# Performance work log

Hardware: AMD Instinct MI355X
Metric: run time of the kernel (lower is better)

## Reference

```python
import jax, jax.numpy as jnp
import numpy as np

B, T, D, BOT = 4, 4096, 2048, 256


def setup_inputs() -> dict:
    key = jax.random.key(0)
    k1, k2, k3, k4 = jax.random.split(key, 4)
    return {
        "hdc_chars": jax.random.normal(k1, (B, T, D), dtype=jnp.float32),
        "decay_matrix": jax.random.uniform(k2, (B, T, T), dtype=jnp.float32),
        "Wq": jax.random.normal(k3, (BOT, D), dtype=jnp.float32) * (D ** -0.5),
        "bq": jnp.zeros((BOT,), dtype=jnp.float32),
        "Wk": jax.random.normal(k4, (BOT, D), dtype=jnp.float32) * (D ** -0.5),
        "bk": jnp.zeros((BOT,), dtype=jnp.float32),
    }


def reference(hdc_chars, decay_matrix, Wq, bq, Wk, bk):
    # hdc_chars: [B,T,D]; decay_matrix: [B,T,T]
    bot = Wq.shape[0]
    scale = bot ** -0.5
    q = hdc_chars @ Wq.T + bq          # [B,T,bot]
    k = hdc_chars @ Wk.T + bk          # [B,T,bot]
    scores = jnp.einsum("btc,bsc->bts", q, k) * scale  # [B,T,T]
    t = scores.shape[-1]
    i = jnp.arange(t)[:, None]
    j = jnp.arange(t)[None, :]
    allowed = j <= i - 4               # tril(diagonal=-4): blocks local echo
    scores = jnp.where(allowed, scores, jnp.float32(-65000.0))
    resonance = jax.nn.softmax(scores, axis=-1)
    combined = 0.7 * decay_matrix + 0.3 * resonance
    return combined @ hdc_chars        # [B,T,D]
```

## Files before the change

### kernel.cpp

```cpp
#include <hip/hip_runtime.h>
#include <hip/hip_bf16.h>

#define BB 4
#define TT 4096
#define DD 2048
#define BOTC 256

typedef __bf16 bf16;
typedef __attribute__((ext_vector_type(4))) __bf16 bf16x4;
typedef __attribute__((ext_vector_type(8))) __bf16 bf16x8;
typedef __attribute__((ext_vector_type(4))) float f32x4;

constexpr int BM = 128, BN = 128, BK = 64;

__device__ __forceinline__ void async16(const void* g, bf16* l) {
  __builtin_amdgcn_global_load_lds((const __attribute__((address_space(1))) void*)g,
                                   (__attribute__((address_space(3))) void*)l, 16, 0, 0);
}

#define SBAR asm volatile("s_barrier" ::: "memory")
#define WAIT_LGKM0 asm volatile("s_waitcnt lgkmcnt(0)" ::: "memory")
#define WAIT_VM6 asm volatile("s_waitcnt vmcnt(6)" ::: "memory")
#define WAIT_VM0 asm volatile("s_waitcnt vmcnt(0)" ::: "memory")

template <int EPI>
__global__ __launch_bounds__(256) void gemm_bt(
    const bf16* __restrict__ A, const bf16* __restrict__ Bm, void* __restrict__ Cout,
    const float* __restrict__ bias, int M, int N, int K, int ldA, int ldB,
    long sAb, long sBb, long sCb, float scale) {
  const int b = blockIdx.z;
  const int m0 = blockIdx.y * BM;
  const int n0 = blockIdx.x * BN;
  const int tid = threadIdx.x;
  const int lane = tid & 63;
  const int w = tid >> 6;
  const int wm = (w >> 1) * 64;
  const int wn = (w & 1) * 64;

  if (EPI == 2 && n0 > m0) return;

  __shared__ bf16 As[BM * BK];
  __shared__ bf16 Bs[BN * BK];

  f32x4 acc[4][4] = {};

  const bf16* Arow = A + (size_t)b * sAb + (size_t)m0 * ldA;
  const bf16* Brow = Bm + (size_t)b * sBb + (size_t)n0 * ldB;

  for (int k0 = 0; k0 < K; k0 += BK) {
#pragma unroll
    for (int j = 0; j < 4; ++j) {
      int c = j * 256 + tid;
      int row = c >> 3, kc = c & 7;
      int gk = kc ^ (row & 7);
      async16(Arow + (size_t)row * ldA + k0 + gk * 8, As + (size_t)c * 8);
      async16(Brow + (size_t)row * ldB + k0 + gk * 8, Bs + (size_t)c * 8);
    }
    __syncthreads();
    bf16x8 af[4][2], bfr[4][2];
#pragma unroll
    for (int mi = 0; mi < 4; ++mi)
#pragma unroll
      for (int kk = 0; kk < 2; ++kk) {
        int row = wm + mi * 16 + (lane & 15);
        int kc = kk * 4 + (lane >> 4);
        af[mi][kk] = *(const bf16x8*)(As + ((size_t)row * 8 + (kc ^ (row & 7))) * 8);
      }
#pragma unroll
    for (int ni = 0; ni < 4; ++ni)
#pragma unroll
      for (int kk = 0; kk < 2; ++kk) {
        int row = wn + ni * 16 + (lane & 15);
        int kc = kk * 4 + (lane >> 4);
        bfr[ni][kk] = *(const bf16x8*)(Bs + ((size_t)row * 8 + (kc ^ (row & 7))) * 8);
      }
#pragma unroll
    for (int kk = 0; kk < 2; ++kk)
#pragma unroll
      for (int mi = 0; mi < 4; ++mi)
#pragma unroll
        for (int ni = 0; ni < 4; ++ni)
          acc[mi][ni] = __builtin_amdgcn_mfma_f32_16x16x32_bf16(af[mi][kk], bfr[ni][kk], acc[mi][ni], 0, 0, 0);
    __syncthreads();
  }

  const int lcol = lane & 15;
  const int lrow = (lane >> 4) * 4;

  if (EPI == 1) {
    bf16* C = (bf16*)Cout + (size_t)b * sCb;
#pragma unroll
    for (int mi = 0; mi < 4; ++mi) {
      int rbase = m0 + wm + mi * 16 + lrow;
#pragma unroll
      for (int ni = 0; ni < 4; ++ni) {
        int col = n0 + wn + ni * 16 + lcol;
        float bv = bias[col];
#pragma unroll
        for (int r = 0; r < 4; ++r)
          C[(size_t)(rbase + r) * N + col] = (bf16)(acc[mi][ni][r] + bv);
      }
    }
  } else {
    bf16* C = (bf16*)Cout + (size_t)b * sCb;
#pragma unroll
    for (int mi = 0; mi < 4; ++mi) {
      int rbase = m0 + wm + mi * 16 + lrow;
#pragma unroll
      for (int ni = 0; ni < 4; ++ni) {
        int col = n0 + wn + ni * 16 + lcol;
#pragma unroll
        for (int r = 0; r < 4; ++r) {
          int i = rbase + r;
          float v = acc[mi][ni][r] * scale;
          if (col > i - 4) v = -65000.0f;
          C[(size_t)i * N + col] = (bf16)v;
        }
      }
    }
  }
}

__device__ __forceinline__ void stage_half(const bf16* __restrict__ src, int ld,
                                           bf16* lds, int tid) {
#pragma unroll
  for (int j = 0; j < 2; ++j) {
    int c = j * 512 + tid;
    int row = c >> 3;
    int gk = (c & 7) ^ (row & 7);
    async16(src + (size_t)row * ld + gk * 8, lds + (size_t)c * 8);
  }
}

__device__ __forceinline__ bf16x8 fragrd(const bf16* base, int lr, int kc) {
  return *(const bf16x8*)(base + ((size_t)lr * 8 + (kc ^ (lr & 7))) * 8);
}

__device__ __forceinline__ void load_b4(const bf16* base, int wn, int fr, int fq,
                                        bf16x8 (&bf_)[4][2]) {
#pragma unroll
  for (int ni = 0; ni < 4; ++ni)
#pragma unroll
    for (int kk = 0; kk < 2; ++kk)
      bf_[ni][kk] = fragrd(base, (wn & 1) * 64 + ni * 16 + fr, kk * 4 + fq);
}

__device__ __forceinline__ void load_a4(const bf16* base, int qm, int fr, int fq,
                                        bf16x8 (&a)[4][2]) {
#pragma unroll
  for (int mi = 0; mi < 4; ++mi)
#pragma unroll
    for (int kk = 0; kk < 2; ++kk)
      a[mi][kk] = fragrd(base, qm * 64 + mi * 16 + fr, kk * 4 + fq);
}

__device__ __forceinline__ void mfma_quad(f32x4 (&acc)[8][4], const bf16x8 (&a)[4][2],
                                          const bf16x8 (&bf_)[4][2], int qm, int qn) {
  __builtin_amdgcn_s_setprio(1);
#pragma unroll
  for (int kk = 0; kk < 2; ++kk)
#pragma unroll
    for (int mi = 0; mi < 4; ++mi)
#pragma unroll
      for (int ni = 0; ni < 2; ++ni)
        acc[qm * 4 + mi][qn * 2 + ni] = __builtin_amdgcn_mfma_f32_16x16x32_bf16(
            a[mi][kk], bf_[qn * 2 + ni][kk], acc[qm * 4 + mi][qn * 2 + ni], 0, 0, 0);
  __builtin_amdgcn_s_setprio(0);
}

__global__ __launch_bounds__(512, 2) void gemm256(
    const bf16* __restrict__ A, const bf16* __restrict__ Bm, float* __restrict__ C,
    int N, int K, int ldA, int ldB, long sAb, long sBb, long sCb) {
  const int h = blockIdx.x + 8 * (blockIdx.y + 16 * blockIdx.z);
  const int l = ((h & 7) << 6) + (h >> 3);
  const int bx = l & 7;
  const int lt = l >> 3;
  const int by = lt & 15;
  const int b = lt >> 4;
  const int m0 = by * 256;
  const int n0 = bx * 256;
  const int tid = threadIdx.x;
  const int lane = tid & 63;
  const int w = tid >> 6;
  const int wm = w >> 2;
  const int wn = w & 3;
  const int fr = lane & 15;
  const int fq = lane >> 4;
  const int bh = wn >> 1;
  const int NKT = K >> 6;
  const int NI = K >> 7;

  __shared__ bf16 sA[2][2][8192];
  __shared__ bf16 sB[2][2][8192];

  const bf16* Ab = A + (size_t)b * sAb + (size_t)m0 * ldA;
  const bf16* Bb = Bm + (size_t)b * sBb + (size_t)n0 * ldB;

  f32x4 acc[8][4] = {};
  bf16x8 a[4][2], bf_[4][2];

  stage_half(Bb, ldB, &sB[0][0][0], tid);
  stage_half(Bb + (size_t)128 * ldB, ldB, &sB[0][1][0], tid);
  stage_half(Ab, ldA, &sA[0][0][0], tid);
  stage_half(Ab + (size_t)128 * ldA, ldA, &sA[0][1][0], tid);
  stage_half(Bb + 64, ldB, &sB[1][0][0], tid);
  stage_half(Bb + (size_t)128 * ldB + 64, ldB, &sB[1][1][0], tid);
  stage_half(Ab + 64, ldA, &sA[1][0][0], tid);
  WAIT_VM6;
  SBAR;

  for (int i = 0; i < NI; ++i) {
    const size_t kA1 = (size_t)(2 * i + 1) * 64;
    int t2 = 2 * i + 2; if (t2 > NKT - 1) t2 = NKT - 1;
    int t3 = 2 * i + 3; if (t3 > NKT - 1) t3 = NKT - 1;
    const size_t k2 = (size_t)t2 * 64, k3 = (size_t)t3 * 64;

    load_b4(&sB[0][bh][0], wn, fr, fq, bf_);
    load_a4(&sA[0][wm][0], 0, fr, fq, a);
    stage_half(Ab + (size_t)128 * ldA + kA1, ldA, &sA[1][1][0], tid);
    SBAR; WAIT_LGKM0; __builtin_amdgcn_sched_barrier(0);
    mfma_quad(acc, a, bf_, 0, 0);
    SBAR;
    stage_half(Bb + k2, ldB, &sB[0][0][0], tid);
    SBAR;
    mfma_quad(acc, a, bf_, 0, 1);
    SBAR;
    load_a4(&sA[0][wm][0], 1, fr, fq, a);
    stage_half(Bb + (size_t)128 * ldB + k2, ldB, &sB[0][1][0], tid);
    SBAR; WAIT_LGKM0; __builtin_amdgcn_sched_barrier(0);
    mfma_quad(acc, a, bf_, 1, 0);
    SBAR;
    stage_half(Ab + k2, ldA, &sA[0][0][0], tid);
    SBAR;
    mfma_quad(acc, a, bf_, 1, 1);
    WAIT_VM6;
    SBAR;
    load_b4(&sB[1][bh][0], wn, fr, fq, bf_);
    load_a4(&sA[1][wm][0], 0, fr, fq, a);
    stage_half(Ab + (size_t)128 * ldA + k2, ldA, &sA[0][1][0], tid);
    SBAR; WAIT_LGKM0; __builtin_amdgcn_sched_barrier(0);
    mfma_quad(acc, a, bf_, 0, 0);
    SBAR;
    stage_half(Bb + k3, ldB, &sB[1][0][0], tid);
    SBAR;
    mfma_quad(acc, a, bf_, 0, 1);
    SBAR;
    load_a4(&sA[1][wm][0], 1, fr, fq, a);
    stage_half(Bb + (size_t)128 * ldB + k3, ldB, &sB[1][1][0], tid);
    SBAR; WAIT_LGKM0; __builtin_amdgcn_sched_barrier(0);
    mfma_quad(acc, a, bf_, 1, 0);
    SBAR;
    stage_half(Ab + k3, ldA, &sA[1][0][0], tid);
    SBAR;
    mfma_quad(acc, a, bf_, 1, 1);
    WAIT_VM6;
    SBAR;
  }

  WAIT_VM0;

  float* Cb = C + (size_t)b * sCb;
  const int lrow = fq * 4;
#pragma unroll
  for (int mi = 0; mi < 8; ++mi) {
    int rbase = m0 + wm * 128 + mi * 16 + lrow;
#pragma unroll
    for (int ni = 0; ni < 4; ++ni) {
      int col = n0 + wn * 64 + ni * 16 + fr;
#pragma unroll
      for (int r = 0; r < 4; ++r)
        Cb[(size_t)(rbase + r) * N + col] = acc[mi][ni][r];
    }
  }
}

__global__ __launch_bounds__(256) void conv_transpose(
    const float* __restrict__ hdc, bf16* __restrict__ hb, bf16* __restrict__ hT) {
  __shared__ float tile[64][65];
  int b = blockIdx.z;
  int d0 = blockIdx.x * 64, t0 = blockIdx.y * 64;
  int tid = threadIdx.x;
  const float* src = hdc + (size_t)b * TT * DD;
  bf16* dstb = hb + (size_t)b * TT * DD;
  bf16* dstT = hT + (size_t)b * DD * TT;
  int c4 = tid & 15, r0 = tid >> 4;
#pragma unroll
  for (int rr = 0; rr < 4; ++rr) {
    int r = rr * 16 + r0;
    float4 v = *(const float4*)(src + (size_t)(t0 + r) * DD + d0 + c4 * 4);
    tile[r][c4 * 4 + 0] = v.x;
    tile[r][c4 * 4 + 1] = v.y;
    tile[r][c4 * 4 + 2] = v.z;
    tile[r][c4 * 4 + 3] = v.w;
    bf16x4 o;
    o[0] = (bf16)v.x; o[1] = (bf16)v.y; o[2] = (bf16)v.z; o[3] = (bf16)v.w;
    *(bf16x4*)(dstb + (size_t)(t0 + r) * DD + d0 + c4 * 4) = o;
  }
  __syncthreads();
  int tc = tid & 7, dr0 = tid >> 3;
#pragma unroll
  for (int rr = 0; rr < 2; ++rr) {
    int dr = rr * 32 + dr0;
    bf16x8 o;
#pragma unroll
    for (int e = 0; e < 8; ++e) o[e] = (bf16)tile[tc * 8 + e][dr];
    *(bf16x8*)(dstT + (size_t)(d0 + dr) * TT + t0 + tc * 8) = o;
  }
}

__global__ __launch_bounds__(256) void conv_w(
    const float* __restrict__ Wq, const float* __restrict__ Wk,
    const float* __restrict__ bq, const float* __restrict__ bk,
    bf16* __restrict__ Wqkb, float* __restrict__ bqk) {
  int i = blockIdx.x * 256 + threadIdx.x;
  float4 q = *(const float4*)(Wq + (size_t)i * 4);
  float4 k = *(const float4*)(Wk + (size_t)i * 4);
  bf16x4 qo, ko;
  qo[0] = (bf16)q.x; qo[1] = (bf16)q.y; qo[2] = (bf16)q.z; qo[3] = (bf16)q.w;
  ko[0] = (bf16)k.x; ko[1] = (bf16)k.y; ko[2] = (bf16)k.z; ko[3] = (bf16)k.w;
  *(bf16x4*)(Wqkb + (size_t)i * 4) = qo;
  *(bf16x4*)(Wqkb + (size_t)BOTC * DD + (size_t)i * 4) = ko;
  if (blockIdx.x == 0) {
    bqk[threadIdx.x] = bq[threadIdx.x];
    bqk[256 + threadIdx.x] = bk[threadIdx.x];
  }
}

__global__ __launch_bounds__(256) void softmax_combine(
    bf16* __restrict__ S, const float* __restrict__ decay) {
  int b = blockIdx.y, i = blockIdx.x;
  bf16* srow = S + ((size_t)b * TT + i) * TT;
  const float* drow = decay + ((size_t)b * TT + i) * TT;
  int t = threadIdx.x;
  int lane = t & 63, w = t >> 6;
  const int valid = i - 3;
  const int nc = valid > 0 ? (valid + 7) >> 3 : 0;

  float p[2][8];
  float inv = 0.f, pc = 0.f;

  if (valid > 0) {
    float s[2][8];
#pragma unroll
    for (int u = 0; u < 2; ++u) {
      int c = u * 256 + t;
      if (c < nc) {
        bf16x8 sv = *(const bf16x8*)(srow + (size_t)c * 8);
#pragma unroll
        for (int e = 0; e < 8; ++e) {
          int j = c * 8 + e;
          s[u][e] = j < valid ? (float)sv[e] : -INFINITY;
        }
      } else {
#pragma unroll
        for (int e = 0; e < 8; ++e) s[u][e] = -INFINITY;
      }
    }
    float m = s[0][0];
#pragma unroll
    for (int u = 0; u < 2; ++u)
#pragma unroll
      for (int e = 0; e < 8; ++e) m = fmaxf(m, s[u][e]);
#pragma unroll
    for (int off = 32; off > 0; off >>= 1) m = fmaxf(m, __shfl_xor(m, off));
    __shared__ float redm[4], reds[4];
    if (lane == 0) redm[w] = m;
    __syncthreads();
    m = fmaxf(fmaxf(redm[0], redm[1]), fmaxf(redm[2], redm[3]));

    float sum = 0.f;
#pragma unroll
    for (int u = 0; u < 2; ++u)
#pragma unroll
      for (int e = 0; e < 8; ++e) {
        p[u][e] = __expf(s[u][e] - m);
        sum += p[u][e];
      }
#pragma unroll
    for (int off = 32; off > 0; off >>= 1) sum += __shfl_xor(sum, off);
    if (lane == 0) reds[w] = sum;
    __syncthreads();
    sum = reds[0] + reds[1] + reds[2] + reds[3];
    inv = 0.3f / sum;
  } else {
    pc = 0.3f / 4096.0f;
#pragma unroll
    for (int u = 0; u < 2; ++u)
#pragma unroll
      for (int e = 0; e < 8; ++e) p[u][e] = 0.f;
  }

#pragma unroll
  for (int u = 0; u < 2; ++u) {
    int c = u * 256 + t;
    const float4* d4 = (const float4*)(drow + (size_t)c * 8);
    float4 da = d4[0], db = d4[1];
    float pv[8];
#pragma unroll
    for (int e = 0; e < 8; ++e) pv[e] = p[u][e] * inv + pc;
    bf16x8 o;
    o[0] = (bf16)(0.7f * da.x + pv[0]);
    o[1] = (bf16)(0.7f * da.y + pv[1]);
    o[2] = (bf16)(0.7f * da.z + pv[2]);
    o[3] = (bf16)(0.7f * da.w + pv[3]);
    o[4] = (bf16)(0.7f * db.x + pv[4]);
    o[5] = (bf16)(0.7f * db.y + pv[5]);
    o[6] = (bf16)(0.7f * db.z + pv[6]);
    o[7] = (bf16)(0.7f * db.w + pv[7]);
    *(bf16x8*)(srow + (size_t)c * 8) = o;
  }
}

extern "C" void kernel_launch(void* const* d_in, const int* in_sizes, int n_in,
                              void* d_out, int out_size, void* d_ws, size_t ws_size,
                              hipStream_t stream) {
  (void)in_sizes; (void)n_in; (void)out_size; (void)ws_size;
  const float* hdc = (const float*)d_in[0];
  const float* decay = (const float*)d_in[1];
  const float* Wq = (const float*)d_in[2];
  const float* bq = (const float*)d_in[3];
  const float* Wk = (const float*)d_in[4];
  const float* bk = (const float*)d_in[5];
  float* out = (float*)d_out;

  char* ws = (char*)d_ws;
  bf16* hdc_b = (bf16*)ws; ws += (size_t)BB * TT * DD * 2;
  bf16* hdcT  = (bf16*)ws; ws += (size_t)BB * TT * DD * 2;
  bf16* Wqkb  = (bf16*)ws; ws += (size_t)2 * BOTC * DD * 2;
  float* bqk  = (float*)ws; ws += 2 * BOTC * 4;
  bf16* qk    = (bf16*)ws; ws += (size_t)BB * TT * 2 * BOTC * 2;
  bf16* S     = (bf16*)ws; ws += (size_t)BB * TT * TT * 2;

  conv_transpose<<<dim3(DD / 64, TT / 64, BB), 256, 0, stream>>>(hdc, hdc_b, hdcT);
  conv_w<<<dim3(BOTC * DD / 1024), 256, 0, stream>>>(Wq, Wk, bq, bk, Wqkb, bqk);

  gemm_bt<1><<<dim3((2 * BOTC) / BN, (BB * TT) / BM, 1), 256, 0, stream>>>(
      hdc_b, Wqkb, qk, bqk, BB * TT, 2 * BOTC, DD, DD, DD, 0, 0, 0, 1.0f);

  gemm_bt<2><<<dim3(TT / BN, TT / BM, BB), 256, 0, stream>>>(
      qk, qk + BOTC, S, nullptr, TT, TT, BOTC, 2 * BOTC, 2 * BOTC,
      (long)TT * 2 * BOTC, (long)TT * 2 * BOTC, (long)TT * TT, 0.0625f);

  softmax_combine<<<dim3(TT, BB), 256, 0, stream>>>(S, decay);

  gemm256<<<dim3(DD / 256, TT / 256, BB), 512, 0, stream>>>(
      S, hdcT, out, DD, TT, TT, TT,
      (long)TT * TT, (long)DD * TT, (long)TT * DD);
}
```

Measured before the change: 882.0 us.

## Split B fragment loads into halves and reorder LDS staging schedule in gemm256

Replaces the single 4-fragment B register load with two 2-fragment loads (bq0/bq1) interleaved between MFMA quads. This lowers register pressure and spreads LDS reads across the loop. The async global-to-LDS staging order is reshuffled so that A tiles are prefetched ahead and B tiles are staged inside the iteration, and the vmcnt wait threshold changes from 6 to 4. The aim is better overlap of LDS reads and global loads with MFMA work, at the risk of extra barriers or stalls, or of a hazard if a stage overwrites a buffer still being read.

```diff
diff --git a/kernel.cpp b/kernel.cpp
--- a/kernel.cpp
+++ b/kernel.cpp
@@ -20,7 +20,8 @@
 
 #define SBAR asm volatile("s_barrier" ::: "memory")
 #define WAIT_LGKM0 asm volatile("s_waitcnt lgkmcnt(0)" ::: "memory")
-#define WAIT_VM6 asm volatile("s_waitcnt vmcnt(6)" ::: "memory")
+#define LGKM_HINT8 asm volatile("s_waitcnt lgkmcnt(8)" ::: "memory")
+#define WAIT_VM4 asm volatile("s_waitcnt vmcnt(4)" ::: "memory")
 #define WAIT_VM0 asm volatile("s_waitcnt vmcnt(0)" ::: "memory")
 
 template <int EPI>
@@ -136,13 +137,13 @@
   return *(const bf16x8*)(base + ((size_t)lr * 8 + (kc ^ (lr & 7))) * 8);
 }
 
-__device__ __forceinline__ void load_b4(const bf16* base, int wn, int fr, int fq,
-                                        bf16x8 (&bf_)[4][2]) {
-#pragma unroll
-  for (int ni = 0; ni < 4; ++ni)
+__device__ __forceinline__ void load_b2(const bf16* base, int wn, int fr, int fq,
+                                        int qn, bf16x8 (&bq)[2][2]) {
+#pragma unroll
+  for (int ni = 0; ni < 2; ++ni)
 #pragma unroll
     for (int kk = 0; kk < 2; ++kk)
-      bf_[ni][kk] = fragrd(base, (wn & 1) * 64 + ni * 16 + fr, kk * 4 + fq);
+      bq[ni][kk] = fragrd(base, (wn & 1) * 64 + (qn * 2 + ni) * 16 + fr, kk * 4 + fq);
 }
 
 __device__ __forceinline__ void load_a4(const bf16* base, int qm, int fr, int fq,
@@ -155,7 +156,7 @@
 }
 
 __device__ __forceinline__ void mfma_quad(f32x4 (&acc)[8][4], const bf16x8 (&a)[4][2],
-                                          const bf16x8 (&bf_)[4][2], int qm, int qn) {
+                                          const bf16x8 (&bq)[2][2], int qm, int qn) {
   __builtin_amdgcn_s_setprio(1);
 #pragma unroll
   for (int kk = 0; kk < 2; ++kk)
@@ -164,7 +165,7 @@
 #pragma unroll
       for (int ni = 0; ni < 2; ++ni)
         acc[qm * 4 + mi][qn * 2 + ni] = __builtin_amdgcn_mfma_f32_16x16x32_bf16(
-            a[mi][kk], bf_[qn * 2 + ni][kk], acc[qm * 4 + mi][qn * 2 + ni], 0, 0, 0);
+            a[mi][kk], bq[ni][kk], acc[qm * 4 + mi][qn * 2 + ni], 0, 0, 0);
   __builtin_amdgcn_s_setprio(0);
 }
 
@@ -197,63 +198,66 @@
   const bf16* Bb = Bm + (size_t)b * sBb + (size_t)n0 * ldB;
 
   f32x4 acc[8][4] = {};
-  bf16x8 a[4][2], bf_[4][2];
+  bf16x8 a[4][2], bq0[2][2], bq1[2][2];
 
   stage_half(Bb, ldB, &sB[0][0][0], tid);
   stage_half(Bb + (size_t)128 * ldB, ldB, &sB[0][1][0], tid);
   stage_half(Ab, ldA, &sA[0][0][0], tid);
   stage_half(Ab + (size_t)128 * ldA, ldA, &sA[0][1][0], tid);
-  stage_half(Bb + 64, ldB, &sB[1][0][0], tid);
-  stage_half(Bb + (size_t)128 * ldB + 64, ldB, &sB[1][1][0], tid);
   stage_half(Ab + 64, ldA, &sA[1][0][0], tid);
-  WAIT_VM6;
+  stage_half(Ab + (size_t)128 * ldA + 64, ldA, &sA[1][1][0], tid);
+  WAIT_VM4;
   SBAR;
 
   for (int i = 0; i < NI; ++i) {
-    const size_t kA1 = (size_t)(2 * i + 1) * 64;
+    const size_t k1 = (size_t)(2 * i + 1) * 64;
     int t2 = 2 * i + 2; if (t2 > NKT - 1) t2 = NKT - 1;
     int t3 = 2 * i + 3; if (t3 > NKT - 1) t3 = NKT - 1;
     const size_t k2 = (size_t)t2 * 64, k3 = (size_t)t3 * 64;
 
-    load_b4(&sB[0][bh][0], wn, fr, fq, bf_);
     load_a4(&sA[0][wm][0], 0, fr, fq, a);
-    stage_half(Ab + (size_t)128 * ldA + kA1, ldA, &sA[1][1][0], tid);
-    SBAR; WAIT_LGKM0; __builtin_amdgcn_sched_barrier(0);
-    mfma_quad(acc, a, bf_, 0, 0);
-    SBAR;
+    load_b2(&sB[0][bh][0], wn, fr, fq, 0, bq0);
+    stage_half(Bb + k1, ldB, &sB[1][0][0], tid);
+    LGKM_HINT8;
+    SBAR; WAIT_LGKM0; __builtin_amdgcn_sched_barrier(0);
+    mfma_quad(acc, a, bq0, 0, 0);
+    SBAR;
+    load_b2(&sB[0][bh][0], wn, fr, fq, 1, bq1);
+    stage_half(Bb + (size_t)128 * ldB + k1, ldB, &sB[1][1][0], tid);
+    SBAR; WAIT_LGKM0; __builtin_amdgcn_sched_barrier(0);
+    mfma_quad(acc, a, bq1, 0, 1);
+    SBAR;
+    load_a4(&sA[0][wm][0], 1, fr, fq, a);
     stage_half(Bb + k2, ldB, &sB[0][0][0], tid);
-    SBAR;
-    mfma_quad(acc, a, bf_, 0, 1);
-    SBAR;
-    load_a4(&sA[0][wm][0], 1, fr, fq, a);
+    SBAR; WAIT_LGKM0; __builtin_amdgcn_sched_barrier(0);
+    mfma_quad(acc, a, bq0, 1, 0);
+    SBAR;
     stage_half(Bb + (size_t)128 * ldB + k2, ldB, &sB[0][1][0], tid);
-    SBAR; WAIT_LGKM0; __builtin_amdgcn_sched_barrier(0);
-    mfma_quad(acc, a, bf_, 1, 0);
-    SBAR;
+    SBAR;
+    mfma_quad(acc, a, bq1, 1, 1);
+    WAIT_VM4;
+    SBAR;
+    load_a4(&sA[1][wm][0], 0, fr, fq, a);
+    load_b2(&sB[1][bh][0], wn, fr, fq, 0, bq0);
     stage_half(Ab + k2, ldA, &sA[0][0][0], tid);
-    SBAR;
-    mfma_quad(acc, a, bf_, 1, 1);
-    WAIT_VM6;
-    SBAR;
-    load_b4(&sB[1][bh][0], wn, fr, fq, bf_);
-    load_a4(&sA[1][wm][0], 0, fr, fq, a);
+    LGKM_HINT8;
+    SBAR; WAIT_LGKM0; __builtin_amdgcn_sched_barrier(0);
+    mfma_quad(acc, a, bq0, 0, 0);
+    SBAR;
+    load_b2(&sB[1][bh][0], wn, fr, fq, 1, bq1);
     stage_half(Ab + (size_t)128 * ldA + k2, ldA, &sA[0][1][0], tid);
     SBAR; WAIT_LGKM0; __builtin_amdgcn_sched_barrier(0);
-    mfma_quad(acc, a, bf_, 0, 0);
-    SBAR;
-    stage_half(Bb + k3, ldB, &sB[1][0][0], tid);
-    SBAR;
-    mfma_quad(acc, a, bf_, 0, 1);
+    mfma_quad(acc, a, bq1, 0, 1);
     SBAR;
     load_a4(&sA[1][wm][0], 1, fr, fq, a);
-    stage_half(Bb + (size_t)128 * ldB + k3, ldB, &sB[1][1][0], tid);
-    SBAR; WAIT_LGKM0; __builtin_amdgcn_sched_barrier(0);
-    mfma_quad(acc, a, bf_, 1, 0);
+    SBAR; WAIT_LGKM0; __builtin_amdgcn_sched_barrier(0);
+    mfma_quad(acc, a, bq0, 1, 0);
     SBAR;
     stage_half(Ab + k3, ldA, &sA[1][0][0], tid);
-    SBAR;
-    mfma_quad(acc, a, bf_, 1, 1);
-    WAIT_VM6;
+    stage_half(Ab + (size_t)128 * ldA + k3, ldA, &sA[1][1][0], tid);
+    SBAR;
+    mfma_quad(acc, a, bq1, 1, 1);
+    WAIT_VM4;
     SBAR;
   }
 
```

Measured after the change: 929.2 us. 5.4% more time.
